# Optimization experiments

Measured on AMD Instinct MI355X. Metric: run time of the kernel, lower is better.

Reference implementation:

```python
import jax, jax.numpy as jnp
import numpy as np

N_NODES = 50000


def _inv_sqrt_deg(idx, n):
    # degree per node from an edge-endpoint index vector; 0-degree -> norm 0 (DGL behavior)
    deg = jax.ops.segment_sum(jnp.ones(idx.shape[0], jnp.float32), idx, num_segments=n)
    return jnp.where(deg > 0, jax.lax.rsqrt(jnp.maximum(deg, 1.0)), 0.0)


def _graph_conv(x, src, dst, W, b, norm_src, norm_dst, n):
    # DGL GraphConv, norm='both': D_dst^{-1/2} A D_src^{-1/2} X W + b
    h = (x * norm_src[:, None]) @ W            # [N, out]
    agg = jax.ops.segment_sum(h[src], dst, num_segments=n)  # SpMM via gather+scatter-add
    return agg * norm_dst[:, None] + b


def setup_inputs() -> dict:
    key = jax.random.key(0)
    ks = jax.random.split(key, 8)
    N, E, D, H, C = N_NODES, 800000, 64, 64, 10
    s = 1.0 / np.sqrt(H)
    return {
        "x": jax.random.normal(ks[0], (N, D), jnp.float32),
        "src": jax.random.randint(ks[1], (E,), 0, N, jnp.int32),
        "dst": jax.random.randint(ks[2], (E,), 0, N, jnp.int32),
        "W1": jax.random.normal(ks[3], (D, H), jnp.float32) * s,
        "b1": jnp.zeros((H,), jnp.float32),
        "W2": jax.random.normal(ks[4], (H, H), jnp.float32) * s,
        "b2": jnp.zeros((H,), jnp.float32),
        "W3": jax.random.normal(ks[5], (H, H), jnp.float32) * s,
        "b3": jnp.zeros((H,), jnp.float32),
        "Wfc": jax.random.normal(ks[6], (H, C), jnp.float32) * s,
        "bfc": jnp.zeros((C,), jnp.float32),
    }


def reference(x, src, dst, W1, b1, W2, b2, W3, b3, Wfc, bfc):
    n = x.shape[0]
    norm_src = _inv_sqrt_deg(src, n)  # out-degree^{-1/2}
    norm_dst = _inv_sqrt_deg(dst, n)  # in-degree^{-1/2}
    h = jnp.tanh(_graph_conv(x, src, dst, W1, b1, norm_src, norm_dst, n))
    h = jnp.tanh(_graph_conv(h, src, dst, W2, b2, norm_src, norm_dst, n))
    h = jnp.tanh(_graph_conv(h, src, dst, W3, b3, norm_src, norm_dst, n))
    return h @ Wfc + bfc
```

## Files before the change

kernel.cpp:

```cpp
#include <hip/hip_runtime.h>
#include <hip/hip_fp16.h>
#include <math.h>

#define THREADS 256
#define CHUNK_SHIFT 15
#define CHUNK (1 << CHUNK_SHIFT)
#define LDS_WORDS 12500
#define MAXB 16
#define XS_STRIDE 68

__global__ __launch_bounds__(1024)
void k_hist(const int* __restrict__ src, const int* __restrict__ dst,
            unsigned int* __restrict__ partS, unsigned int* __restrict__ partD,
            unsigned char* __restrict__ rank, unsigned int* __restrict__ counter,
            int E, int P, int words) {
    __shared__ unsigned int hist[LDS_WORDS];
    if (blockIdx.x == 0 && threadIdx.x == 0) *counter = 0u;
    int isSrc = (blockIdx.x >= (unsigned)P);
    int b = isSrc ? (blockIdx.x - P) : blockIdx.x;
    int tid = threadIdx.x;

    for (int w = tid; w < words; w += 1024) hist[w] = 0u;
    __syncthreads();

    int start = b << CHUNK_SHIFT;
    int end = start + CHUNK; if (end > E) end = E;

    if (isSrc) {
        for (int e = start + tid; e < end; e += 1024) {
            int s = src[e];
            atomicAdd(&hist[s >> 2], 1u << ((s & 3) * 8));
        }
    } else {
        for (int e = start + tid; e < end; e += 1024) {
            int d = dst[e];
            unsigned int old = atomicAdd(&hist[d >> 2], 1u << ((d & 3) * 8));
            rank[e] = (unsigned char)((old >> ((d & 3) * 8)) & 0xFFu);
        }
    }
    __syncthreads();

    unsigned int* part = isSrc ? partS : partD;
    for (int w = tid; w < words; w += 1024)
        part[(size_t)b * words + w] = hist[w];
}

__global__ __launch_bounds__(THREADS)
void k_pre(const unsigned int* __restrict__ partS,
           const unsigned int* __restrict__ partD,
           unsigned int* __restrict__ prefD,
           int* __restrict__ deg_d, float* __restrict__ ns, float* __restrict__ nd,
           int* __restrict__ rp, int* __restrict__ bsum,
           unsigned int* __restrict__ counter,
           int P, int words, int N) {
    __shared__ unsigned int qsD[4][64];
    __shared__ unsigned int qsS[4][64];
    int t = threadIdx.x;
    int widx = t & 63;
    int q = t >> 6;
    int w = blockIdx.x * 64 + widx;
    bool valid = (w < words);

    int per = (P + 3) >> 2;
    int blo = q * per;
    int cnt = P - blo; if (cnt > per) cnt = per; if (cnt < 0) cnt = 0;

    unsigned int vD[MAXB];
    unsigned int runD = 0, runS = 0;
#pragma unroll
    for (int bb = 0; bb < MAXB; bb++) {
        unsigned int vd = 0, vs = 0;
        if (bb < cnt && valid) {
            size_t off = (size_t)(blo + bb) * words + w;
            vd = partD[off];
            vs = partS[off];
        }
        vD[bb] = vd;
        runD += vd;
        runS += vs;
    }
    qsD[q][widx] = runD;
    qsS[q][widx] = runS;
    __syncthreads();

    unsigned int baseD = 0, totD = 0, totS = 0;
#pragma unroll
    for (int qq = 0; qq < 4; qq++) {
        unsigned int xd = qsD[qq][widx];
        unsigned int xs = qsS[qq][widx];
        if (qq < q) baseD += xd;
        totD += xd;
        totS += xs;
    }

    unsigned int pref = baseD;
#pragma unroll
    for (int bb = 0; bb < MAXB; bb++) {
        if (bb < cnt && valid)
            prefD[(size_t)(blo + bb) * words + w] = pref;
        pref += vD[bb];
    }

    if (q == 0) {
        int b0 = (int)(totD & 0xFFu), b1 = (int)((totD >> 8) & 0xFFu),
            b2 = (int)((totD >> 16) & 0xFFu), b3 = (int)((totD >> 24) & 0xFFu);
        int wsum = b0 + b1 + b2 + b3;
        int incl = wsum;
#pragma unroll
        for (int off = 1; off < 64; off <<= 1) {
            int y = __shfl_up(incl, off);
            if (widx >= off) incl += y;
        }
        int excl = incl - wsum;
        int btot = __shfl(incl, 63);
        if (widx == 0)
            bsum[blockIdx.x] = (int)atomicAdd(counter, (unsigned int)btot);
        if (valid) {
            int s0 = (int)(totS & 0xFFu), s1 = (int)((totS >> 8) & 0xFFu),
                s2 = (int)((totS >> 16) & 0xFFu), s3 = (int)((totS >> 24) & 0xFFu);
            int4 dv; dv.x = b0; dv.y = b1; dv.z = b2; dv.w = b3;
            *(int4*)&deg_d[(size_t)4 * w] = dv;
            float4 ndv;
            ndv.x = b0 ? 1.0f / sqrtf((float)b0) : 0.0f;
            ndv.y = b1 ? 1.0f / sqrtf((float)b1) : 0.0f;
            ndv.z = b2 ? 1.0f / sqrtf((float)b2) : 0.0f;
            ndv.w = b3 ? 1.0f / sqrtf((float)b3) : 0.0f;
            *(float4*)&nd[(size_t)4 * w] = ndv;
            float4 nsv;
            nsv.x = s0 ? 1.0f / sqrtf((float)s0) : 0.0f;
            nsv.y = s1 ? 1.0f / sqrtf((float)s1) : 0.0f;
            nsv.z = s2 ? 1.0f / sqrtf((float)s2) : 0.0f;
            nsv.w = s3 ? 1.0f / sqrtf((float)s3) : 0.0f;
            *(float4*)&ns[(size_t)4 * w] = nsv;
            int4 rv; rv.x = excl; rv.y = excl + b0;
            rv.z = excl + b0 + b1; rv.w = excl + b0 + b1 + b2;
            *(int4*)&rp[(size_t)4 * w] = rv;
        }
    }
}

__global__ __launch_bounds__(256, 4)
void k_fill_gemm(const int* __restrict__ src, const int* __restrict__ dst,
                 const int* __restrict__ rp, const int* __restrict__ bsum,
                 const unsigned char* __restrict__ rank,
                 const unsigned int* __restrict__ prefD,
                 int* __restrict__ col, int E, int words, int gFill,
                 const float* __restrict__ X, const float* __restrict__ norm,
                 const float* __restrict__ W, __half* __restrict__ H, int N) {
    __shared__ float Xs[64 * XS_STRIDE];
    __shared__ float Ws[64 * 64];
    int tid = threadIdx.x;

    if ((int)blockIdx.x < gFill) {
        int e = blockIdx.x * 256 + tid;
        if (e < E) {
            int d = dst[e];
            int b = e >> CHUNK_SHIFT;
            unsigned int pk = prefD[(size_t)b * words + (d >> 2)];
            int pref = (int)((pk >> ((d & 3) * 8)) & 0xFFu);
            col[rp[d] + bsum[d >> 8] + pref + (int)rank[e]] = src[e];
        }
        return;
    }

    int rowBase = ((int)blockIdx.x - gFill) * 64;
    for (int i = tid; i < 1024; i += 256)
        ((float4*)Ws)[i] = ((const float4*)W)[i];
    for (int i = tid; i < 1024; i += 256) {
        int r = i >> 4, k4 = i & 15;
        int row = rowBase + r;
        float4 v = make_float4(0.f, 0.f, 0.f, 0.f);
        if (row < N) {
            v = ((const float4*)X)[(size_t)row * 16 + k4];
            float nv = norm[row];
            v.x *= nv; v.y *= nv; v.z *= nv; v.w *= nv;
        }
        *((float4*)&Xs[r * XS_STRIDE + (k4 << 2)]) = v;
    }
    __syncthreads();

    int tc = tid & 15, tr = tid >> 4;
    int c0 = tc * 4, r0 = tr * 4;
    float acc[4][4] = {};

#pragma unroll 2
    for (int k = 0; k < 64; k += 4) {
        float4 wv[4];
#pragma unroll
        for (int kk = 0; kk < 4; kk++)
            wv[kk] = *((const float4*)&Ws[(k + kk) * 64 + c0]);
#pragma unroll
        for (int j = 0; j < 4; j++) {
            float4 xv = *((const float4*)&Xs[(r0 + j) * XS_STRIDE + k]);
            acc[j][0] += xv.x * wv[0].x; acc[j][1] += xv.x * wv[0].y;
            acc[j][2] += xv.x * wv[0].z; acc[j][3] += xv.x * wv[0].w;
            acc[j][0] += xv.y * wv[1].x; acc[j][1] += xv.y * wv[1].y;
            acc[j][2] += xv.y * wv[1].z; acc[j][3] += xv.y * wv[1].w;
            acc[j][0] += xv.z * wv[2].x; acc[j][1] += xv.z * wv[2].y;
            acc[j][2] += xv.z * wv[2].z; acc[j][3] += xv.z * wv[2].w;
            acc[j][0] += xv.w * wv[3].x; acc[j][1] += xv.w * wv[3].y;
            acc[j][2] += xv.w * wv[3].z; acc[j][3] += xv.w * wv[3].w;
        }
    }
#pragma unroll
    for (int j = 0; j < 4; j++) {
        int row = rowBase + r0 + j;
        if (row < N) {
            __half2 h01 = __floats2half2_rn(acc[j][0], acc[j][1]);
            __half2 h23 = __floats2half2_rn(acc[j][2], acc[j][3]);
            uint2 pk;
            pk.x = *(unsigned int*)&h01;
            pk.y = *(unsigned int*)&h23;
            *((uint2*)(H + (size_t)row * 64 + c0)) = pk;
        }
    }
}

template<int FC>
__global__ __launch_bounds__(512)
void k_agg_gemm(const uint4* __restrict__ H4, const int* __restrict__ rp,
                const int* __restrict__ bsum, const int* __restrict__ deg,
                const int* __restrict__ col, const float* __restrict__ nd,
                const float* __restrict__ nsrc, const float* __restrict__ bias,
                const float* __restrict__ W, const float* __restrict__ Wb2,
                void* __restrict__ OutP, int N) {
    __shared__ float Xs[64 * XS_STRIDE];
    __shared__ float Ws[FC ? 680 : 4096];
    __shared__ float Wb[16];
    int tid = threadIdx.x;

    if constexpr (FC == 0) {
        for (int i = tid; i < 1024; i += 512)
            ((float4*)Ws)[i] = ((const float4*)W)[i];
    } else {
        for (int i = tid; i < 640; i += 512) {
            int k = i / 10, c = i - k * 10;
            Ws[c * 68 + k] = W[i];
        }
        if (tid < 10) Wb[tid] = Wb2[tid];
    }
    __syncthreads();

    int wave = tid >> 6;
    int lane = tid & 63;
    int g = lane >> 3;
    int l = lane & 7;
    int rowBase = blockIdx.x * 64;
    int row = wave * 8 + g;

    float4 bv0 = *((const float4*)&bias[l * 8]);
    float4 bv1 = *((const float4*)&bias[l * 8 + 4]);

    int node = rowBase + row;
    int st = 0, n = 0; float nv = 0.f, nsv = 0.f;
    if (node < N) {
        st  = rp[node] + bsum[node >> 8];
        n   = deg[node];
        nv  = nd[node];
        if constexpr (FC == 0) nsv = nsrc[node];
    }
    int idx = (l < n) ? col[st + l] : 0;

    int m = n;
#pragma unroll
    for (int d = 8; d <= 32; d <<= 1) {
        int tm = __shfl_xor(m, d); m = m > tm ? m : tm;
    }

    {
        float acc[8] = {0.f, 0.f, 0.f, 0.f, 0.f, 0.f, 0.f, 0.f};
        for (int j0 = 0; j0 < m; j0 += 8) {
            int idxn = ((j0 + 8 + l) < n) ? col[st + j0 + 8 + l] : 0;
#pragma unroll
            for (int jj = 0; jj < 8; jj++) {
                int s = __shfl(idx, (g << 3) + jj);
                if (j0 + jj < n) {
                    uint4 v = H4[(size_t)s * 8 + l];
                    float2 f0 = __half22float2(*(__half2*)&v.x);
                    float2 f1 = __half22float2(*(__half2*)&v.y);
                    float2 f2 = __half22float2(*(__half2*)&v.z);
                    float2 f3 = __half22float2(*(__half2*)&v.w);
                    acc[0] += f0.x; acc[1] += f0.y; acc[2] += f1.x; acc[3] += f1.y;
                    acc[4] += f2.x; acc[5] += f2.y; acc[6] += f3.x; acc[7] += f3.y;
                }
            }
            idx = idxn;
        }
        float4 o0, o1;
        o0.x = tanhf(acc[0] * nv + bv0.x);
        o0.y = tanhf(acc[1] * nv + bv0.y);
        o0.z = tanhf(acc[2] * nv + bv0.z);
        o0.w = tanhf(acc[3] * nv + bv0.w);
        o1.x = tanhf(acc[4] * nv + bv1.x);
        o1.y = tanhf(acc[5] * nv + bv1.y);
        o1.z = tanhf(acc[6] * nv + bv1.z);
        o1.w = tanhf(acc[7] * nv + bv1.w);
        if constexpr (FC == 0) {
            o0.x *= nsv; o0.y *= nsv; o0.z *= nsv; o0.w *= nsv;
            o1.x *= nsv; o1.y *= nsv; o1.z *= nsv; o1.w *= nsv;
        }
        if (node >= N) {
            o0 = make_float4(0.f, 0.f, 0.f, 0.f);
            o1 = make_float4(0.f, 0.f, 0.f, 0.f);
        }
        *((float4*)&Xs[row * XS_STRIDE + l * 8])     = o0;
        *((float4*)&Xs[row * XS_STRIDE + l * 8 + 4]) = o1;
    }

    if constexpr (FC == 0) {
        __half* Hh = (__half*)OutP;
        float a2[8] = {0.f, 0.f, 0.f, 0.f, 0.f, 0.f, 0.f, 0.f};
#pragma unroll 2
        for (int k = 0; k < 64; k += 4) {
            float4 xv = *((const float4*)&Xs[row * XS_STRIDE + k]);
#pragma unroll
            for (int kk = 0; kk < 4; kk++) {
                float4 w0 = *((const float4*)&Ws[(k + kk) * 64 + l * 8]);
                float4 w1 = *((const float4*)&Ws[(k + kk) * 64 + l * 8 + 4]);
                float xk = (kk == 0) ? xv.x : (kk == 1) ? xv.y : (kk == 2) ? xv.z : xv.w;
                a2[0] += xk * w0.x; a2[1] += xk * w0.y;
                a2[2] += xk * w0.z; a2[3] += xk * w0.w;
                a2[4] += xk * w1.x; a2[5] += xk * w1.y;
                a2[6] += xk * w1.z; a2[7] += xk * w1.w;
            }
        }
        int grow = rowBase + row;
        if (grow < N) {
            __half2 h0 = __floats2half2_rn(a2[0], a2[1]);
            __half2 h1 = __floats2half2_rn(a2[2], a2[3]);
            __half2 h2 = __floats2half2_rn(a2[4], a2[5]);
            __half2 h3 = __floats2half2_rn(a2[6], a2[7]);
            uint4 pk;
            pk.x = *(unsigned int*)&h0;
            pk.y = *(unsigned int*)&h1;
            pk.z = *(unsigned int*)&h2;
            pk.w = *(unsigned int*)&h3;
            *((uint4*)(Hh + (size_t)grow * 64 + l * 8)) = pk;
        }
    } else {
        float* outF = (float*)OutP;
        for (int t2 = lane; t2 < 80; t2 += 64) {
            int ln = t2 / 10;
            int cl = t2 - ln * 10;
            int lrow = wave * 8 + ln;
            float acc = Wb[cl];
#pragma unroll
            for (int k = 0; k < 64; k += 4) {
                float4 xv = *((const float4*)&Xs[lrow * XS_STRIDE + k]);
                float4 wv = *((const float4*)&Ws[cl * 68 + k]);
                acc += xv.x * wv.x + xv.y * wv.y + xv.z * wv.z + xv.w * wv.w;
            }
            int grow = rowBase + lrow;
            if (grow < N) outF[(size_t)grow * 10 + cl] = acc;
        }
    }
}

extern "C" void kernel_launch(void* const* d_in, const int* in_sizes, int n_in,
                              void* d_out, int out_size, void* d_ws, size_t ws_size,
                              hipStream_t stream) {
    const float* x   = (const float*)d_in[0];
    const int*   src = (const int*)d_in[1];
    const int*   dst = (const int*)d_in[2];
    const float* W1  = (const float*)d_in[3];
    const float* b1  = (const float*)d_in[4];
    const float* W2  = (const float*)d_in[5];
    const float* b2  = (const float*)d_in[6];
    const float* W3  = (const float*)d_in[7];
    const float* b3  = (const float*)d_in[8];
    const float* Wfc = (const float*)d_in[9];
    const float* bfc = (const float*)d_in[10];
    float* out = (float*)d_out;
    int N = in_sizes[0] / 64;
    int E = in_sizes[1];
    int P = (E + CHUNK - 1) >> CHUNK_SHIFT;
    int words = (N + 3) / 4;

    char* ws = (char*)d_ws;
    size_t p = 0;
    auto alloc = [&](size_t bytes) -> void* {
        void* r = ws + p;
        p = (p + bytes + 255) & ~(size_t)255;
        return r;
    };
    int*    deg_d = (int*)alloc((size_t)N * 4);
    int*    rp    = (int*)alloc((size_t)N * 4);
    int*    bsum  = (int*)alloc((size_t)THREADS * 4);
    unsigned char* rank = (unsigned char*)alloc((size_t)E);
    int*    col   = (int*)alloc((size_t)E * 4);
    float*  ns    = (float*)alloc((size_t)N * 4);
    float*  nd    = (float*)alloc((size_t)N * 4);
    unsigned int* partS = (unsigned int*)alloc((size_t)P * words * 4);
    unsigned int* partD = (unsigned int*)alloc((size_t)P * words * 4);
    unsigned int* prefD = (unsigned int*)alloc((size_t)P * words * 4);
    __half* bufH  = (__half*)alloc((size_t)N * 64 * 2);
    __half* bufH2 = (__half*)alloc((size_t)N * 64 * 2);
    unsigned int* counter = (unsigned int*)alloc(4);
    (void)ws_size; (void)n_in; (void)out_size;

    int gFill = (E + 255) / 256;
    int gP = (words + 63) / 64;
    int gGemm = (N + 63) / 64;
    int gAgg  = (N + 63) / 64;

    k_hist<<<2 * P, 1024, 0, stream>>>(src, dst, partS, partD, rank, counter, E, P, words);
    k_pre <<<gP, THREADS, 0, stream>>>(partS, partD, prefD, deg_d, ns, nd,
                                       rp, bsum, counter, P, words, N);
    k_fill_gemm<<<gFill + gGemm, 256, 0, stream>>>(src, dst, rp, bsum, rank, prefD,
                                                   col, E, words, gFill,
                                                   x, ns, W1, bufH, N);
    k_agg_gemm<0><<<gAgg, 512, 0, stream>>>((const uint4*)bufH,  rp, bsum, deg_d, col,
                                            nd, ns, b1, W2, nullptr, bufH2, N);
    k_agg_gemm<0><<<gAgg, 512, 0, stream>>>((const uint4*)bufH2, rp, bsum, deg_d, col,
                                            nd, ns, b2, W3, nullptr, bufH, N);
    k_agg_gemm<1><<<gAgg, 512, 0, stream>>>((const uint4*)bufH,  rp, bsum, deg_d, col,
                                            nd, ns, b3, Wfc, bfc, out, N);
}
```

Before: 187.6 us.

## Move first-layer GEMM into histogram kernel and defer source-norm scaling

The first-layer X·W1 product now runs inside the histogram launch as extra 1024-thread blocks. This is allowed because diag(ns)·X·W equals diag(ns)·(X·W), so the GEMM no longer has to wait for the degree norms. It writes an fp32 intermediate, and the fill kernel later scales it by the source norm and converts it to half. The aim is to overlap the dense GEMM with the histogram pass. In exchange it adds an extra fp32 N×64 buffer that is written and read back, and the GEMM blocks are 1024 threads with one output per thread, which is less efficient.

```diff
diff --git a/kernel.cpp b/kernel.cpp
--- a/kernel.cpp
+++ b/kernel.cpp
@@ -10,39 +10,80 @@
 #define XS_STRIDE 68
 
 __global__ __launch_bounds__(1024)
-void k_hist(const int* __restrict__ src, const int* __restrict__ dst,
-            unsigned int* __restrict__ partS, unsigned int* __restrict__ partD,
-            unsigned char* __restrict__ rank, unsigned int* __restrict__ counter,
-            int E, int P, int words) {
-    __shared__ unsigned int hist[LDS_WORDS];
-    if (blockIdx.x == 0 && threadIdx.x == 0) *counter = 0u;
-    int isSrc = (blockIdx.x >= (unsigned)P);
-    int b = isSrc ? (blockIdx.x - P) : blockIdx.x;
+void k_hist_gemm(const int* __restrict__ src, const int* __restrict__ dst,
+                 unsigned int* __restrict__ partS, unsigned int* __restrict__ partD,
+                 unsigned char* __restrict__ rank, unsigned int* __restrict__ counter,
+                 int E, int P, int words,
+                 const float* __restrict__ X, const float* __restrict__ W,
+                 float* __restrict__ G, int N) {
+    __shared__ unsigned int lds_u[LDS_WORDS];
     int tid = threadIdx.x;
-
-    for (int w = tid; w < words; w += 1024) hist[w] = 0u;
+    int b = blockIdx.x;
+
+    if (b < 2 * P) {
+        unsigned int* hist = lds_u;
+        if (b == 0 && tid == 0) *counter = 0u;
+        int isSrc = (b >= P);
+        int cb = isSrc ? (b - P) : b;
+
+        for (int w = tid; w < words; w += 1024) hist[w] = 0u;
+        __syncthreads();
+
+        int start = cb << CHUNK_SHIFT;
+        int end = start + CHUNK; if (end > E) end = E;
+
+        if (isSrc) {
+            for (int e = start + tid; e < end; e += 1024) {
+                int s = src[e];
+                atomicAdd(&hist[s >> 2], 1u << ((s & 3) * 8));
+            }
+        } else {
+            for (int e = start + tid; e < end; e += 1024) {
+                int d = dst[e];
+                unsigned int old = atomicAdd(&hist[d >> 2], 1u << ((d & 3) * 8));
+                rank[e] = (unsigned char)((old >> ((d & 3) * 8)) & 0xFFu);
+            }
+        }
+        __syncthreads();
+
+        unsigned int* part = isSrc ? partS : partD;
+        for (int w = tid; w < words; w += 1024)
+            part[(size_t)cb * words + w] = hist[w];
+        return;
+    }
+
+    float* Xs = (float*)lds_u;
+    float* Ws = ((float*)lds_u) + 64 * XS_STRIDE;
+    int rowBase = (b - 2 * P) * 64;
+
+    ((float4*)Ws)[tid] = ((const float4*)W)[tid];
+    {
+        int r = tid >> 4, k4 = tid & 15;
+        int row = rowBase + r;
+        float4 v = make_float4(0.f, 0.f, 0.f, 0.f);
+        if (row < N) v = ((const float4*)X)[(size_t)row * 16 + k4];
+        *((float4*)&Xs[r * XS_STRIDE + (k4 << 2)]) = v;
+    }
     __syncthreads();
 
-    int start = b << CHUNK_SHIFT;
-    int end = start + CHUNK; if (end > E) end = E;
-
-    if (isSrc) {
-        for (int e = start + tid; e < end; e += 1024) {
-            int s = src[e];
-            atomicAdd(&hist[s >> 2], 1u << ((s & 3) * 8));
-        }
-    } else {
-        for (int e = start + tid; e < end; e += 1024) {
-            int d = dst[e];
-            unsigned int old = atomicAdd(&hist[d >> 2], 1u << ((d & 3) * 8));
-            rank[e] = (unsigned char)((old >> ((d & 3) * 8)) & 0xFFu);
-        }
-    }
-    __syncthreads();
-
-    unsigned int* part = isSrc ? partS : partD;
-    for (int w = tid; w < words; w += 1024)
-        part[(size_t)b * words + w] = hist[w];
+    int tc = tid & 15, tr = tid >> 4;
+    int c0 = tc * 4;
+    float a0 = 0.f, a1 = 0.f, a2 = 0.f, a3 = 0.f;
+#pragma unroll 4
+    for (int k = 0; k < 64; k += 4) {
+        float4 xv = *((const float4*)&Xs[tr * XS_STRIDE + k]);
+        float4 w0 = *((const float4*)&Ws[(k + 0) * 64 + c0]);
+        float4 w1 = *((const float4*)&Ws[(k + 1) * 64 + c0]);
+        float4 w2 = *((const float4*)&Ws[(k + 2) * 64 + c0]);
+        float4 w3 = *((const float4*)&Ws[(k + 3) * 64 + c0]);
+        a0 += xv.x * w0.x; a1 += xv.x * w0.y; a2 += xv.x * w0.z; a3 += xv.x * w0.w;
+        a0 += xv.y * w1.x; a1 += xv.y * w1.y; a2 += xv.y * w1.z; a3 += xv.y * w1.w;
+        a0 += xv.z * w2.x; a1 += xv.z * w2.y; a2 += xv.z * w2.z; a3 += xv.z * w2.w;
+        a0 += xv.w * w3.x; a1 += xv.w * w3.y; a2 += xv.w * w3.z; a3 += xv.w * w3.w;
+    }
+    int row = rowBase + tr;
+    if (row < N)
+        *((float4*)&G[(size_t)row * 64 + c0]) = make_float4(a0, a1, a2, a3);
 }
 
 __global__ __launch_bounds__(THREADS)
@@ -139,18 +180,15 @@
     }
 }
 
-__global__ __launch_bounds__(256, 4)
-void k_fill_gemm(const int* __restrict__ src, const int* __restrict__ dst,
-                 const int* __restrict__ rp, const int* __restrict__ bsum,
-                 const unsigned char* __restrict__ rank,
-                 const unsigned int* __restrict__ prefD,
-                 int* __restrict__ col, int E, int words, int gFill,
-                 const float* __restrict__ X, const float* __restrict__ norm,
-                 const float* __restrict__ W, __half* __restrict__ H, int N) {
-    __shared__ float Xs[64 * XS_STRIDE];
-    __shared__ float Ws[64 * 64];
+__global__ __launch_bounds__(256)
+void k_fill_scale(const int* __restrict__ src, const int* __restrict__ dst,
+                  const int* __restrict__ rp, const int* __restrict__ bsum,
+                  const unsigned char* __restrict__ rank,
+                  const unsigned int* __restrict__ prefD,
+                  int* __restrict__ col, int E, int words, int gFill,
+                  const float* __restrict__ G, const float* __restrict__ norm,
+                  __half* __restrict__ H, int N) {
     int tid = threadIdx.x;
-
     if ((int)blockIdx.x < gFill) {
         int e = blockIdx.x * 256 + tid;
         if (e < E) {
@@ -162,57 +200,18 @@
         }
         return;
     }
-
-    int rowBase = ((int)blockIdx.x - gFill) * 64;
-    for (int i = tid; i < 1024; i += 256)
-        ((float4*)Ws)[i] = ((const float4*)W)[i];
-    for (int i = tid; i < 1024; i += 256) {
-        int r = i >> 4, k4 = i & 15;
-        int row = rowBase + r;
-        float4 v = make_float4(0.f, 0.f, 0.f, 0.f);
-        if (row < N) {
-            v = ((const float4*)X)[(size_t)row * 16 + k4];
-            float nv = norm[row];
-            v.x *= nv; v.y *= nv; v.z *= nv; v.w *= nv;
-        }
-        *((float4*)&Xs[r * XS_STRIDE + (k4 << 2)]) = v;
-    }
-    __syncthreads();
-
-    int tc = tid & 15, tr = tid >> 4;
-    int c0 = tc * 4, r0 = tr * 4;
-    float acc[4][4] = {};
-
-#pragma unroll 2
-    for (int k = 0; k < 64; k += 4) {
-        float4 wv[4];
-#pragma unroll
-        for (int kk = 0; kk < 4; kk++)
-            wv[kk] = *((const float4*)&Ws[(k + kk) * 64 + c0]);
-#pragma unroll
-        for (int j = 0; j < 4; j++) {
-            float4 xv = *((const float4*)&Xs[(r0 + j) * XS_STRIDE + k]);
-            acc[j][0] += xv.x * wv[0].x; acc[j][1] += xv.x * wv[0].y;
-            acc[j][2] += xv.x * wv[0].z; acc[j][3] += xv.x * wv[0].w;
-            acc[j][0] += xv.y * wv[1].x; acc[j][1] += xv.y * wv[1].y;
-            acc[j][2] += xv.y * wv[1].z; acc[j][3] += xv.y * wv[1].w;
-            acc[j][0] += xv.z * wv[2].x; acc[j][1] += xv.z * wv[2].y;
-            acc[j][2] += xv.z * wv[2].z; acc[j][3] += xv.z * wv[2].w;
-            acc[j][0] += xv.w * wv[3].x; acc[j][1] += xv.w * wv[3].y;
-            acc[j][2] += xv.w * wv[3].z; acc[j][3] += xv.w * wv[3].w;
-        }
-    }
-#pragma unroll
-    for (int j = 0; j < 4; j++) {
-        int row = rowBase + r0 + j;
-        if (row < N) {
-            __half2 h01 = __floats2half2_rn(acc[j][0], acc[j][1]);
-            __half2 h23 = __floats2half2_rn(acc[j][2], acc[j][3]);
-            uint2 pk;
-            pk.x = *(unsigned int*)&h01;
-            pk.y = *(unsigned int*)&h23;
-            *((uint2*)(H + (size_t)row * 64 + c0)) = pk;
-        }
+    int i = ((int)blockIdx.x - gFill) * 256 + tid;
+    if (i < N * 16) {
+        int row = i >> 4;
+        int k4 = i & 15;
+        float nv = norm[row];
+        float4 v = ((const float4*)G)[i];
+        __half2 h01 = __floats2half2_rn(v.x * nv, v.y * nv);
+        __half2 h23 = __floats2half2_rn(v.z * nv, v.w * nv);
+        uint2 pk;
+        pk.x = *(unsigned int*)&h01;
+        pk.y = *(unsigned int*)&h23;
+        *((uint2*)(H + (size_t)row * 64 + (k4 << 2))) = pk;
     }
 }
 
@@ -395,20 +394,24 @@
     unsigned int* prefD = (unsigned int*)alloc((size_t)P * words * 4);
     __half* bufH  = (__half*)alloc((size_t)N * 64 * 2);
     __half* bufH2 = (__half*)alloc((size_t)N * 64 * 2);
+    float*  bufG  = (float*)alloc((size_t)N * 64 * 4);
     unsigned int* counter = (unsigned int*)alloc(4);
     (void)ws_size; (void)n_in; (void)out_size;
 
-    int gFill = (E + 255) / 256;
-    int gP = (words + 63) / 64;
-    int gGemm = (N + 63) / 64;
-    int gAgg  = (N + 63) / 64;
-
-    k_hist<<<2 * P, 1024, 0, stream>>>(src, dst, partS, partD, rank, counter, E, P, words);
+    int gFill  = (E + 255) / 256;
+    int gP     = (words + 63) / 64;
+    int gGemm  = (N + 63) / 64;
+    int gScale = (N * 16 + 255) / 256;
+    int gAgg   = (N + 63) / 64;
+
+    k_hist_gemm<<<2 * P + gGemm, 1024, 0, stream>>>(src, dst, partS, partD, rank,
+                                                    counter, E, P, words,
+                                                    x, W1, bufG, N);
     k_pre <<<gP, THREADS, 0, stream>>>(partS, partD, prefD, deg_d, ns, nd,
                                        rp, bsum, counter, P, words, N);
-    k_fill_gemm<<<gFill + gGemm, 256, 0, stream>>>(src, dst, rp, bsum, rank, prefD,
-                                                   col, E, words, gFill,
-                                                   x, ns, W1, bufH, N);
+    k_fill_scale<<<gFill + gScale, 256, 0, stream>>>(src, dst, rp, bsum, rank, prefD,
+                                                     col, E, words, gFill,
+                                                     bufG, ns, bufH, N);
     k_agg_gemm<0><<<gAgg, 512, 0, stream>>>((const uint4*)bufH,  rp, bsum, deg_d, col,
                                             nd, ns, b1, W2, nullptr, bufH2, N);
     k_agg_gemm<0><<<gAgg, 512, 0, stream>>>((const uint4*)bufH2, rp, bsum, deg_d, col,
```

After: 185.4 us. No clear change (-1.2%).
